# Kernel optimization log

Measured on AMD Instinct MI355X. Metric: run time of the kernel, lower is better.

The kernel has to match this reference:

```python
import jax, jax.numpy as jnp
import numpy as np
from jax import lax

B, L, D = 2, 1024, 1024
EXPAND, N, K = 2, 16, 4          # expand, d_state, d_conv
DI = EXPAND * D                  # d_inner = 2048
R = (D + 15) // 16               # dt_rank = 64
EPS = 1e-5


def setup_inputs() -> dict:
    key = jax.random.key(0)
    ks = jax.random.split(key, 8)
    x = jax.random.normal(ks[0], (B, L, D), dtype=jnp.float32)
    ln_w = jnp.ones((D,), jnp.float32)
    ln_b = jnp.zeros((D,), jnp.float32)
    W_in = jax.random.normal(ks[1], (D, 2 * DI), jnp.float32) * (1.0 / np.sqrt(D))
    conv_w = jax.random.normal(ks[2], (DI, K), jnp.float32) * 0.2
    conv_b = jnp.zeros((DI,), jnp.float32)
    W_x = jax.random.normal(ks[3], (DI, R + 2 * N), jnp.float32) * (1.0 / np.sqrt(DI))
    W_dt = jax.random.normal(ks[4], (R, DI), jnp.float32) * (1.0 / np.sqrt(R))
    b_dt = jnp.full((DI,), -4.0, jnp.float32)  # softplus(-4) ~ 0.018 dt init
    A_log = jnp.log(jnp.broadcast_to(jnp.arange(1, N + 1, dtype=jnp.float32), (DI, N)))
    D_param = jnp.ones((DI,), jnp.float32)
    W_out = jax.random.normal(ks[5], (DI, D), jnp.float32) * (1.0 / np.sqrt(DI))
    return {"x": x, "ln_w": ln_w, "ln_b": ln_b, "W_in": W_in, "conv_w": conv_w,
            "conv_b": conv_b, "W_x": W_x, "W_dt": W_dt, "b_dt": b_dt,
            "A_log": A_log, "D_param": D_param, "W_out": W_out}


def _mamba_block(x, ln_w, ln_b, W_in, conv_w, conv_b, W_x, W_dt, b_dt, A_log, D_param, W_out):
    # pre-LayerNorm
    mu = jnp.mean(x, axis=-1, keepdims=True)
    xc = x - mu
    var = jnp.mean(xc * xc, axis=-1, keepdims=True)
    h = xc * lax.rsqrt(var + EPS) * ln_w + ln_b          # [B,L,D]

    xz = h @ W_in                                        # [B,L,2*DI]
    xi, z = xz[..., :DI], xz[..., DI:]

    # depthwise causal conv1d, kernel K, left pad K-1
    xp = jnp.pad(xi, ((0, 0), (K - 1, 0), (0, 0)))
    conv = conv_b
    for k in range(K):
        conv = conv + xp[:, k:k + L, :] * conv_w[:, k]
    u = jax.nn.silu(conv)                                # [B,L,DI]

    proj = u @ W_x                                       # [B,L,R+2N]
    dt_r = proj[..., :R]
    Bm = proj[..., R:R + N]                              # [B,L,N]
    Cm = proj[..., R + N:]                               # [B,L,N]
    dt = jax.nn.softplus(dt_r @ W_dt + b_dt)             # [B,L,DI]

    A = -jnp.exp(A_log)                                  # [DI,N]
    dA = jnp.exp(dt[..., None] * A)                      # [B,L,DI,N]
    dBu = (dt * u)[..., None] * Bm[:, :, None, :]        # [B,L,DI,N]

    def comb(e1, e2):
        a1, b1 = e1
        a2, b2 = e2
        return a1 * a2, a2 * b1 + b2

    _, hs = lax.associative_scan(comb, (dA, dBu), axis=1)  # [B,L,DI,N]
    y = jnp.einsum('bldn,bln->bld', hs, Cm) + u * D_param
    y = y * jax.nn.silu(z)
    return x + y @ W_out


def reference(x, ln_w, ln_b, W_in, conv_w, conv_b, W_x, W_dt, b_dt, A_log, D_param, W_out):
    return _mamba_block(x, ln_w, ln_b, W_in, conv_w, conv_b, W_x, W_dt, b_dt,
                        A_log, D_param, W_out)
```

## Files before the change

kernel.cpp:

```cpp
#include <hip/hip_runtime.h>
#include <hip/hip_bf16.h>
#include <math.h>

#define B_ 2
#define L_ 1024
#define D_ 1024
#define DI_ 2048
#define K_ 4
#define N_ 16
#define R_ 64
#define BL_ (B_ * L_)
#define EPS_ 1e-5f

#define IDX4(l) ((l) + (((l) >> 6) << 2))

typedef __attribute__((ext_vector_type(8))) short short8;
typedef __attribute__((ext_vector_type(4))) float f32x4;

__device__ inline unsigned short f2bf(float f) {
    unsigned u = __float_as_uint(f);
    unsigned r = (u + 0x7fffu + ((u >> 16) & 1u)) >> 16;
    return (unsigned short)r;
}
__device__ inline float bf2f(unsigned short s) {
    return __uint_as_float(((unsigned)s) << 16);
}
__device__ inline float fast_silu(float z) {
    return z * __builtin_amdgcn_rcpf(1.f + __expf(-z));
}
__device__ inline void gl_lds16(const void* g, void* l) {
    __builtin_amdgcn_global_load_lds(
        (const __attribute__((address_space(1))) void*)g,
        (__attribute__((address_space(3))) void*)l, 16, 0, 0);
}

template <int CTRL>
__device__ inline float dpp_shr(float x) {
    return __int_as_float(__builtin_amdgcn_update_dpp(
        0, __float_as_int(x), CTRL, 0xf, 0xf, true));
}
__device__ inline float row16_sum(float p) {
    p += dpp_shr<0x111>(p);
    p += dpp_shr<0x112>(p);
    p += dpp_shr<0x114>(p);
    p += dpp_shr<0x118>(p);
    return p;
}

__global__ void ln_kernel(const float* __restrict__ x, const float* __restrict__ w,
                          const float* __restrict__ b, unsigned short* __restrict__ hb) {
    int row = blockIdx.x;
    const float* xr = x + (size_t)row * D_;
    float4 v = ((const float4*)xr)[threadIdx.x];

    __shared__ float red[4];
    float s = v.x + v.y + v.z + v.w;
    for (int off = 1; off < 64; off <<= 1) s += __shfl_xor(s, off, 64);
    if ((threadIdx.x & 63) == 0) red[threadIdx.x >> 6] = s;
    __syncthreads();
    float mu = (red[0] + red[1] + red[2] + red[3]) * (1.0f / D_);
    __syncthreads();
    float cx = v.x - mu, cy = v.y - mu, cz = v.z - mu, cw = v.w - mu;
    float sq = cx*cx + cy*cy + cz*cz + cw*cw;
    for (int off = 1; off < 64; off <<= 1) sq += __shfl_xor(sq, off, 64);
    if ((threadIdx.x & 63) == 0) red[threadIdx.x >> 6] = sq;
    __syncthreads();
    float var = (red[0] + red[1] + red[2] + red[3]) * (1.0f / D_);
    float rstd = rsqrtf(var + EPS_);

    float4 wv = ((const float4*)w)[threadIdx.x];
    float4 bv = ((const float4*)b)[threadIdx.x];
    ushort4 o;
    o.x = f2bf(cx * rstd * wv.x + bv.x);
    o.y = f2bf(cy * rstd * wv.y + bv.y);
    o.z = f2bf(cz * rstd * wv.z + bv.z);
    o.w = f2bf(cw * rstd * wv.w + bv.w);
    ((ushort4*)(hb + (size_t)row * D_))[threadIdx.x] = o;
}

__global__ void transpose_cast_all(const float* __restrict__ W_in, const float* __restrict__ W_x,
                                   const float* __restrict__ W_out,
                                   unsigned short* __restrict__ WinT, unsigned short* __restrict__ WxT,
                                   unsigned short* __restrict__ WoutT) {
    int bid = blockIdx.x;
    const float* W; unsigned short* WT; int K, N, bx, by;
    if (bid < 4096)      { W = W_in;  WT = WinT;  K = 1024; N = 4096; bx = bid & 127; by = bid >> 7; }
    else if (bid < 4288) { int id = bid - 4096; W = W_x;  WT = WxT;  K = DI_; N = 96;   bx = id % 3;  by = id / 3; }
    else                 { int id = bid - 4288; W = W_out; WT = WoutT; K = DI_; N = 1024; bx = id & 31; by = id >> 5; }
    __shared__ float tile[32][33];
    int k0 = by * 32, n0 = bx * 32;
    int tr = threadIdx.x >> 5;
    int tc = threadIdx.x & 31;
#pragma unroll
    for (int i = 0; i < 4; ++i)
        tile[tr + i*8][tc] = W[(size_t)(k0 + tr + i*8) * N + n0 + tc];
    __syncthreads();
#pragma unroll
    for (int i = 0; i < 4; ++i)
        WT[(size_t)(n0 + tr + i*8) * K + k0 + tc] = f2bf(tile[tc][tr + i*8]);
}

template <int BN, int MODE>
__global__ __launch_bounds__(256) void mfma_gemm_bt(
        const unsigned short* __restrict__ A,  int lda,
        const unsigned short* __restrict__ BT, int ldb,
        float* __restrict__ C, int ldc, int Kchunk,
        float* __restrict__ xi, unsigned short* __restrict__ sz) {
    constexpr int NT = BN / 32;
    __shared__ unsigned short As[128 * 32];
    __shared__ unsigned short Bs[BN * 32];

    int tid = threadIdx.x;
    int wave = tid >> 6, lane = tid & 63;
    int lane15 = lane & 15, quad = lane >> 4;
    int wr = wave >> 1, wc = wave & 1;

    int m0 = blockIdx.y * 128;
    int n0 = blockIdx.x * BN;
    int kbeg = blockIdx.z * Kchunk;
    int kend = kbeg + Kchunk;

    f32x4 acc[4][NT];
#pragma unroll
    for (int i = 0; i < 4; ++i)
#pragma unroll
        for (int j = 0; j < NT; ++j) acc[i][j] = (f32x4){0.f, 0.f, 0.f, 0.f};

    constexpr int ACALLS = 8;
    constexpr int BCALLS = BN * 4 / 64;

    for (int k0 = kbeg; k0 < kend; k0 += 32) {
        __syncthreads();
        for (int c = wave; c < ACALLS + BCALLS; c += 4) {
            if (c < ACALLS) {
                int cell = c * 64 + lane;
                int m = cell >> 2, s = cell & 3;
                int q = s ^ (m & 3) ^ ((m >> 2) & 3);
                gl_lds16(A + (size_t)(m0 + m) * lda + k0 + q * 8, &As[c * 512]);
            } else {
                int cell = (c - ACALLS) * 64 + lane;
                int n = cell >> 2, s = cell & 3;
                int q = s ^ (n & 3) ^ ((n >> 2) & 3);
                gl_lds16(BT + (size_t)(n0 + n) * ldb + k0 + q * 8, &Bs[(c - ACALLS) * 512]);
            }
        }
        __syncthreads();

        short8 af[4], bfr[NT];
#pragma unroll
        for (int i = 0; i < 4; ++i) {
            int m = wr * 64 + i * 16 + lane15;
            int s = quad ^ (m & 3) ^ ((m >> 2) & 3);
            af[i] = *(const short8*)&As[m * 32 + s * 8];
        }
#pragma unroll
        for (int j = 0; j < NT; ++j) {
            int n = wc * (NT * 16) + j * 16 + lane15;
            int s = quad ^ (n & 3) ^ ((n >> 2) & 3);
            bfr[j] = *(const short8*)&Bs[n * 32 + s * 8];
        }
#pragma unroll
        for (int i = 0; i < 4; ++i)
#pragma unroll
            for (int j = 0; j < NT; ++j)
                acc[i][j] = __builtin_amdgcn_mfma_f32_16x16x32_bf16(af[i], bfr[j], acc[i][j], 0, 0, 0);
    }

#pragma unroll
    for (int i = 0; i < 4; ++i) {
        int row = m0 + wr * 64 + i * 16 + quad * 4;
#pragma unroll
        for (int j = 0; j < NT; ++j) {
            int col = n0 + wc * (NT * 16) + j * 16 + lane15;
#pragma unroll
            for (int r = 0; r < 4; ++r) {
                float v = acc[i][j][r];
                int rr = row + r;
                if (MODE == 0) {
                    C[(size_t)rr * ldc + col] = v;
                } else if (MODE == 1) {
                    atomicAdd(&C[(size_t)rr * ldc + col], v);
                } else {
                    if (col < DI_) xi[(size_t)rr * DI_ + col] = v;
                    else           sz[(size_t)rr * DI_ + (col - DI_)] = f2bf(fast_silu(v));
                }
            }
        }
    }
}

__global__ void conv_silu_kernel(const float* __restrict__ xi, const float* __restrict__ cw,
                                 const float* __restrict__ cb, unsigned short* __restrict__ ub) {
    int idx = blockIdx.x * blockDim.x + threadIdx.x;
    int c = idx & (DI_ - 1);
    int bl = idx >> 11;
    int l = bl & (L_ - 1);
    float4 w4 = ((const float4*)cw)[c];
    float acc = cb[c];
    const float* base = xi + (size_t)bl * DI_ + c;
    if (l >= 3) {
        acc = fmaf(base[-(size_t)3 * DI_], w4.x, acc);
        acc = fmaf(base[-(size_t)2 * DI_], w4.y, acc);
        acc = fmaf(base[-(size_t)1 * DI_], w4.z, acc);
        acc = fmaf(base[0],                w4.w, acc);
    } else {
        if (l >= 2) acc = fmaf(*(base - 2 * DI_), w4.y, acc);
        if (l >= 1) acc = fmaf(*(base - 1 * DI_), w4.z, acc);
        acc = fmaf(base[0], w4.w, acc);
    }
    ub[idx] = f2bf(fast_silu(acc));
}

__global__ __launch_bounds__(256) void dtprep(
        const float* __restrict__ proj, const float* __restrict__ W_dt,
        const float* __restrict__ b_dt, const unsigned short* __restrict__ ub,
        const unsigned short* __restrict__ szb, const float* __restrict__ Dp,
        float2* __restrict__ dtduT, unsigned int* __restrict__ szdT) {
    __shared__ alignas(16) unsigned char smem[64 * 65 * 8];
    float (*As)[68] = reinterpret_cast<float(*)[68]>(smem);
    float (*Bs)[64] = reinterpret_cast<float(*)[64]>(smem + 4352);
    float2 (*T2)[65] = reinterpret_cast<float2(*)[65]>(smem);
    unsigned int (*TU)[65] = reinterpret_cast<unsigned int(*)[65]>(smem);

    int tid = threadIdx.x;
    int n0 = blockIdx.x * 64;
    int m0 = blockIdx.y * 64;
    int ar = tid >> 2, ak = (tid & 3) << 2;
    int kb = tid >> 4, bc = (tid & 15) << 2;
    int ty = tid >> 4, tx = tid & 15;

    float acc[4][4] = {};
#pragma unroll
    for (int k0 = 0; k0 < R_; k0 += 16) {
        float4 av = *(const float4*)&proj[(size_t)(m0 + ar) * 96 + k0 + ak];
        As[ak + 0][ar] = av.x; As[ak + 1][ar] = av.y;
        As[ak + 2][ar] = av.z; As[ak + 3][ar] = av.w;
        float4 bv = *(const float4*)&W_dt[(size_t)(k0 + kb) * DI_ + n0 + bc];
        Bs[kb][bc + 0] = bv.x; Bs[kb][bc + 1] = bv.y;
        Bs[kb][bc + 2] = bv.z; Bs[kb][bc + 3] = bv.w;
        __syncthreads();
#pragma unroll
        for (int kk = 0; kk < 16; ++kk) {
            float a[4], bb[4];
#pragma unroll
            for (int i = 0; i < 4; ++i) a[i] = As[kk][ty * 4 + i];
#pragma unroll
            for (int j = 0; j < 4; ++j) bb[j] = Bs[kk][tx * 4 + j];
#pragma unroll
            for (int i = 0; i < 4; ++i)
#pragma unroll
                for (int j = 0; j < 4; ++j)
                    acc[i][j] = fmaf(a[i], bb[j], acc[i][j]);
        }
        __syncthreads();
    }

    float4 bd = *(const float4*)&b_dt[n0 + tx * 4];
    float4 dp4 = *(const float4*)&Dp[n0 + tx * 4];
    float bda[4] = {bd.x, bd.y, bd.z, bd.w};
    float dpa[4] = {dp4.x, dp4.y, dp4.z, dp4.w};
    float2 d2[4][4];
    unsigned int su[4][4];
#pragma unroll
    for (int i = 0; i < 4; ++i) {
        int bl = m0 + ty * 4 + i;
        ushort4 u4 = *(const ushort4*)&ub[(size_t)bl * DI_ + n0 + tx * 4];
        ushort4 s4 = *(const ushort4*)&szb[(size_t)bl * DI_ + n0 + tx * 4];
        unsigned short ua[4] = {u4.x, u4.y, u4.z, u4.w};
        unsigned short sa[4] = {s4.x, s4.y, s4.z, s4.w};
#pragma unroll
        for (int j = 0; j < 4; ++j) {
            float v = acc[i][j] + bda[j];
            float dtv = fmaxf(v, 0.f) + __logf(1.f + __expf(-fabsf(v)));
            float uu = bf2f(ua[j]);
            float szv = bf2f(sa[j]);
            d2[i][j] = make_float2(dtv, dtv * uu);
            su[i][j] = ((unsigned)f2bf(uu * dpa[j] * szv) << 16) | (unsigned)f2bf(szv);
        }
    }

#pragma unroll
    for (int i = 0; i < 4; ++i)
#pragma unroll
        for (int j = 0; j < 4; ++j)
            T2[ty * 4 + i][tx * 4 + j] = d2[i][j];
    __syncthreads();
#pragma unroll
    for (int i = 0; i < 8; ++i) {
        int c_l = (tid >> 5) + i * 8;
#pragma unroll
        for (int jj = 0; jj < 2; ++jj) {
            int bl_l = (tid & 31) + jj * 32;
            dtduT[(size_t)(n0 + c_l) * BL_ + m0 + bl_l] = T2[bl_l][c_l];
        }
    }
    __syncthreads();

#pragma unroll
    for (int i = 0; i < 4; ++i)
#pragma unroll
        for (int j = 0; j < 4; ++j)
            TU[ty * 4 + i][tx * 4 + j] = su[i][j];
    __syncthreads();
#pragma unroll
    for (int i = 0; i < 8; ++i) {
        int c_l = (tid >> 5) + i * 8;
#pragma unroll
        for (int jj = 0; jj < 2; ++jj) {
            int bl_l = (tid & 31) + jj * 32;
            szdT[(size_t)(n0 + c_l) * BL_ + m0 + bl_l] = TU[bl_l][c_l];
        }
    }
}

__global__ __launch_bounds__(256) void scan_v5(
        const float2* __restrict__ dtduT, const unsigned int* __restrict__ szdT,
        const float* __restrict__ proj, const float* __restrict__ A_log,
        unsigned short* __restrict__ yzT) {
    int bc = blockIdx.x;
    int b = bc >> 10;
    int cp = bc & 1023;
    int t = threadIdx.x;
    int n = t & 15;
    int cs = (t >> 4) & 1;
    int chunk = t >> 5;
    int c = cp * 2 + cs;

    __shared__ float dd[2][(L_ + 32) * 2];
    __shared__ float sA[8][32];
    __shared__ float sB[8][32];
    __shared__ float ps[2][L_ + 64];

    {
        int half = t >> 7;
        int tt = t & 127;
        int l = tt * 8;
        int cload = cp * 2 + half;
        const float4* g = (const float4*)(dtduT + (size_t)cload * BL_ + (size_t)b * L_ + l);
        int il2 = l + ((l >> 6) << 1);
        float* dst = &dd[half][il2 * 2];
        *(float4*)(dst + 0)  = g[0];
        *(float4*)(dst + 4)  = g[1];
        *(float4*)(dst + 8)  = g[2];
        *(float4*)(dst + 12) = g[3];
    }
    __syncthreads();

    float A = -__expf(A_log[c * N_ + n]);
    int l0 = chunk * 128;
    const float* pB = proj + (size_t)b * L_ * 96 + R_ + n;
    const float* pC = pB + N_;

    float a = 1.f, acc = 0.f;
#pragma unroll
    for (int h = 0; h < 2; ++h) {
        int lb = l0 + h * 64;
        const float* ddp = &dd[cs][(lb + ((lb >> 6) << 1)) * 2];
        const float* pBb = pB + (size_t)lb * 96;
#pragma unroll
        for (int q = 0; q < 16; ++q) {
            float4 d0 = *(const float4*)(ddp + q * 8);
            float4 d1 = *(const float4*)(ddp + q * 8 + 4);
            float b0 = pBb[(q*4 + 0) * 96];
            float b1 = pBb[(q*4 + 1) * 96];
            float b2 = pBb[(q*4 + 2) * 96];
            float b3 = pBb[(q*4 + 3) * 96];
            float e;
            e = __expf(d0.x * A); a *= e; acc = fmaf(e, acc, d0.y * b0);
            e = __expf(d0.z * A); a *= e; acc = fmaf(e, acc, d0.w * b1);
            e = __expf(d1.x * A); a *= e; acc = fmaf(e, acc, d1.y * b2);
            e = __expf(d1.z * A); a *= e; acc = fmaf(e, acc, d1.w * b3);
        }
    }
    sA[chunk][t & 31] = a;
    sB[chunk][t & 31] = acc;
    __syncthreads();

    if (t < 32) {
        float hc = 0.f;
#pragma unroll
        for (int j = 0; j < 8; ++j) {
            float aj = sA[j][t];
            float bj = sB[j][t];
            sB[j][t] = hc;
            hc = fmaf(aj, hc, bj);
        }
    }
    __syncthreads();
    float h = sB[chunk][t & 31];

#pragma unroll
    for (int hh = 0; hh < 2; ++hh) {
        int lb = l0 + hh * 64;
        const float* ddp = &dd[cs][(lb + ((lb >> 6) << 1)) * 2];
        const float* pBb = pB + (size_t)lb * 96;
        const float* pCb = pC + (size_t)lb * 96;
        float* psb = &ps[cs][IDX4(lb)];
#pragma unroll
        for (int q = 0; q < 16; ++q) {
            float4 d0 = *(const float4*)(ddp + q * 8);
            float4 d1 = *(const float4*)(ddp + q * 8 + 4);
            float b0 = pBb[(q*4 + 0) * 96], c0 = pCb[(q*4 + 0) * 96];
            float b1 = pBb[(q*4 + 1) * 96], c1 = pCb[(q*4 + 1) * 96];
            float b2 = pBb[(q*4 + 2) * 96], c2 = pCb[(q*4 + 2) * 96];
            float b3 = pBb[(q*4 + 3) * 96], c3 = pCb[(q*4 + 3) * 96];
            float e, p0, p1, p2, p3;
            e = __expf(d0.x * A); h = fmaf(e, h, d0.y * b0); p0 = row16_sum(h * c0);
            e = __expf(d0.z * A); h = fmaf(e, h, d0.w * b1); p1 = row16_sum(h * c1);
            e = __expf(d1.x * A); h = fmaf(e, h, d1.y * b2); p2 = row16_sum(h * c2);
            e = __expf(d1.z * A); h = fmaf(e, h, d1.w * b3); p3 = row16_sum(h * c3);
            if (n == 15) *(float4*)&psb[q * 4] = (float4){p0, p1, p2, p3};
        }
    }
    __syncthreads();

    {
        int half = t >> 7;
        int tt = t & 127;
        int l = tt * 8;
        int c_out = cp * 2 + half;
        size_t tb = (size_t)c_out * BL_ + (size_t)b * L_;
        const float* pp = &ps[half][IDX4(l)];
        ushort4 o[2];
#pragma unroll
        for (int g = 0; g < 2; ++g) {
            float4 p4 = *(const float4*)(pp + g * 4);
            uint4 sd4 = *(const uint4*)(szdT + tb + l + g * 4);
            o[g].x = f2bf(p4.x * bf2f((unsigned short)(sd4.x & 0xffff)) + bf2f((unsigned short)(sd4.x >> 16)));
            o[g].y = f2bf(p4.y * bf2f((unsigned short)(sd4.y & 0xffff)) + bf2f((unsigned short)(sd4.y >> 16)));
            o[g].z = f2bf(p4.z * bf2f((unsigned short)(sd4.z & 0xffff)) + bf2f((unsigned short)(sd4.z >> 16)));
            o[g].w = f2bf(p4.w * bf2f((unsigned short)(sd4.w & 0xffff)) + bf2f((unsigned short)(sd4.w >> 16)));
        }
        *(ushort4*)(yzT + tb + l) = o[0];
        *(ushort4*)(yzT + tb + l + 4) = o[1];
    }
}

__global__ void transpose_y(const unsigned short* __restrict__ yzT, unsigned short* __restrict__ yz) {
    __shared__ unsigned short t[32][33];
    int c0 = blockIdx.y * 32, bl0 = blockIdx.x * 32;
    int r = threadIdx.x >> 5;
    int col = threadIdx.x & 31;
#pragma unroll
    for (int i = 0; i < 4; ++i)
        t[r + i*8][col] = yzT[(size_t)(c0 + r + i*8) * BL_ + bl0 + col];
    __syncthreads();
#pragma unroll
    for (int i = 0; i < 4; ++i)
        yz[(size_t)(bl0 + r + i*8) * DI_ + c0 + col] = t[col][r + i*8];
}

extern "C" void kernel_launch(void* const* d_in, const int* in_sizes, int n_in,
                              void* d_out, int out_size, void* d_ws, size_t ws_size,
                              hipStream_t stream) {
    const float* x       = (const float*)d_in[0];
    const float* ln_w    = (const float*)d_in[1];
    const float* ln_b    = (const float*)d_in[2];
    const float* W_in    = (const float*)d_in[3];
    const float* conv_w  = (const float*)d_in[4];
    const float* conv_b  = (const float*)d_in[5];
    const float* W_x     = (const float*)d_in[6];
    const float* W_dt    = (const float*)d_in[7];
    const float* b_dt    = (const float*)d_in[8];
    const float* A_log   = (const float*)d_in[9];
    const float* D_param = (const float*)d_in[10];
    const float* W_out   = (const float*)d_in[11];
    float* out = (float*)d_out;

    uint8_t* p = (uint8_t*)d_ws;
    unsigned short* hb    = (unsigned short*)p;  p += (size_t)BL_ * D_ * 2;
    unsigned short* WinT  = (unsigned short*)p;  p += (size_t)4096 * 1024 * 2;
    float*          xib   = (float*)p;           p += (size_t)BL_ * DI_ * 4;
    unsigned short* szb   = (unsigned short*)p;  p += (size_t)BL_ * DI_ * 2;
    unsigned short* ub    = (unsigned short*)p;  p += (size_t)BL_ * DI_ * 2;
    unsigned short* WxT   = (unsigned short*)p;  p += (size_t)96 * DI_ * 2;
    float*          proj  = (float*)p;           p += (size_t)BL_ * 96 * 4;
    unsigned short* WoutT = (unsigned short*)p;  p += (size_t)1024 * DI_ * 2;
    float2*         dtduT = (float2*)p;          p += (size_t)BL_ * DI_ * 8;
    unsigned int*   szdT  = (unsigned int*)p;    p += (size_t)BL_ * DI_ * 4;
    unsigned short* yzT   = (unsigned short*)p;  p += (size_t)BL_ * DI_ * 2;
    unsigned short* yzb   = (unsigned short*)d_ws;

    hipMemsetAsync(proj, 0, (size_t)BL_ * 96 * 4, stream);
    hipMemcpyAsync(out, x, (size_t)BL_ * D_ * 4, hipMemcpyDeviceToDevice, stream);

    transpose_cast_all<<<6336, 256, 0, stream>>>(W_in, W_x, W_out, WinT, WxT, WoutT);

    ln_kernel<<<BL_, 256, 0, stream>>>(x, ln_w, ln_b, hb);

    mfma_gemm_bt<128, 3><<<dim3(4096 / 128, BL_ / 128, 1), 256, 0, stream>>>(
        hb, 1024, WinT, 1024, nullptr, 0, 1024, xib, szb);

    conv_silu_kernel<<<(BL_ * DI_) / 256, 256, 0, stream>>>(xib, conv_w, conv_b, ub);

    mfma_gemm_bt<96, 1><<<dim3(1, BL_ / 128, 16), 256, 0, stream>>>(
        ub, DI_, WxT, DI_, proj, 96, 128, nullptr, nullptr);

    dtprep<<<dim3(DI_ / 64, BL_ / 64), 256, 0, stream>>>(
        proj, W_dt, b_dt, ub, szb, D_param, dtduT, szdT);

    scan_v5<<<B_ * DI_ / 2, 256, 0, stream>>>(dtduT, szdT, proj, A_log, yzT);

    transpose_y<<<dim3(BL_ / 32, DI_ / 32), 256, 0, stream>>>(yzT, yzb);

    mfma_gemm_bt<128, 1><<<dim3(1024 / 128, BL_ / 128, 2), 256, 0, stream>>>(
        yzb, DI_, WoutT, DI_, out, 1024, 1024, nullptr, nullptr);
}
```

Baseline: 286.7 us.

## Store conv input as bf16, vectorize conv, interleave B/C, drop scan LDS staging

The in-projection GEMM now writes the conv input xi as bf16 instead of fp32. The conv kernel is vectorized to handle four channels per thread with ushort4 loads. dtprep additionally writes an interleaved B/C buffer, so the scan reads B and C as one float2 instead of two strided proj loads. The scan drops its LDS staging of dt/du and reads directly from global memory. This cuts memory traffic, at the cost of extra bf16 rounding of the conv input and possibly less efficient global access patterns in the scan.

```diff
diff --git a/kernel.cpp b/kernel.cpp
--- a/kernel.cpp
+++ b/kernel.cpp
@@ -105,7 +105,7 @@
         const unsigned short* __restrict__ A,  int lda,
         const unsigned short* __restrict__ BT, int ldb,
         float* __restrict__ C, int ldc, int Kchunk,
-        float* __restrict__ xi, unsigned short* __restrict__ sz) {
+        unsigned short* __restrict__ xi, unsigned short* __restrict__ sz) {
     constexpr int NT = BN / 32;
     __shared__ unsigned short As[128 * 32];
     __shared__ unsigned short Bs[BN * 32];
@@ -181,7 +181,7 @@
                 } else if (MODE == 1) {
                     atomicAdd(&C[(size_t)rr * ldc + col], v);
                 } else {
-                    if (col < DI_) xi[(size_t)rr * DI_ + col] = v;
+                    if (col < DI_) xi[(size_t)rr * DI_ + col] = f2bf(v);
                     else           sz[(size_t)rr * DI_ + (col - DI_)] = f2bf(fast_silu(v));
                 }
             }
@@ -189,33 +189,50 @@
     }
 }
 
-__global__ void conv_silu_kernel(const float* __restrict__ xi, const float* __restrict__ cw,
+__global__ void conv_silu_kernel(const unsigned short* __restrict__ xi, const float* __restrict__ cw,
                                  const float* __restrict__ cb, unsigned short* __restrict__ ub) {
     int idx = blockIdx.x * blockDim.x + threadIdx.x;
-    int c = idx & (DI_ - 1);
-    int bl = idx >> 11;
+    int c4 = (idx << 2) & (DI_ - 1);
+    int bl = (idx << 2) >> 11;
     int l = bl & (L_ - 1);
-    float4 w4 = ((const float4*)cw)[c];
-    float acc = cb[c];
-    const float* base = xi + (size_t)bl * DI_ + c;
+    float4 w0 = ((const float4*)cw)[c4 + 0];
+    float4 w1 = ((const float4*)cw)[c4 + 1];
+    float4 w2 = ((const float4*)cw)[c4 + 2];
+    float4 w3 = ((const float4*)cw)[c4 + 3];
+    float4 cbv = *(const float4*)&cb[c4];
+    float a0 = cbv.x, a1 = cbv.y, a2 = cbv.z, a3 = cbv.w;
+    const unsigned short* base = xi + (size_t)bl * DI_ + c4;
+
+    ushort4 t0 = *(const ushort4*)base;
+    a0 = fmaf(bf2f(t0.x), w0.w, a0); a1 = fmaf(bf2f(t0.y), w1.w, a1);
+    a2 = fmaf(bf2f(t0.z), w2.w, a2); a3 = fmaf(bf2f(t0.w), w3.w, a3);
+    if (l >= 1) {
+        ushort4 t1 = *(const ushort4*)(base - DI_);
+        a0 = fmaf(bf2f(t1.x), w0.z, a0); a1 = fmaf(bf2f(t1.y), w1.z, a1);
+        a2 = fmaf(bf2f(t1.z), w2.z, a2); a3 = fmaf(bf2f(t1.w), w3.z, a3);
+    }
+    if (l >= 2) {
+        ushort4 t2 = *(const ushort4*)(base - 2 * DI_);
+        a0 = fmaf(bf2f(t2.x), w0.y, a0); a1 = fmaf(bf2f(t2.y), w1.y, a1);
+        a2 = fmaf(bf2f(t2.z), w2.y, a2); a3 = fmaf(bf2f(t2.w), w3.y, a3);
+    }
     if (l >= 3) {
-        acc = fmaf(base[-(size_t)3 * DI_], w4.x, acc);
-        acc = fmaf(base[-(size_t)2 * DI_], w4.y, acc);
-        acc = fmaf(base[-(size_t)1 * DI_], w4.z, acc);
-        acc = fmaf(base[0],                w4.w, acc);
-    } else {
-        if (l >= 2) acc = fmaf(*(base - 2 * DI_), w4.y, acc);
-        if (l >= 1) acc = fmaf(*(base - 1 * DI_), w4.z, acc);
-        acc = fmaf(base[0], w4.w, acc);
-    }
-    ub[idx] = f2bf(fast_silu(acc));
+        ushort4 t3 = *(const ushort4*)(base - 3 * DI_);
+        a0 = fmaf(bf2f(t3.x), w0.x, a0); a1 = fmaf(bf2f(t3.y), w1.x, a1);
+        a2 = fmaf(bf2f(t3.z), w2.x, a2); a3 = fmaf(bf2f(t3.w), w3.x, a3);
+    }
+    ushort4 o;
+    o.x = f2bf(fast_silu(a0)); o.y = f2bf(fast_silu(a1));
+    o.z = f2bf(fast_silu(a2)); o.w = f2bf(fast_silu(a3));
+    *(ushort4*)(ub + (size_t)bl * DI_ + c4) = o;
 }
 
 __global__ __launch_bounds__(256) void dtprep(
         const float* __restrict__ proj, const float* __restrict__ W_dt,
         const float* __restrict__ b_dt, const unsigned short* __restrict__ ub,
         const unsigned short* __restrict__ szb, const float* __restrict__ Dp,
-        float2* __restrict__ dtduT, unsigned int* __restrict__ szdT) {
+        float2* __restrict__ dtduT, unsigned int* __restrict__ szdT,
+        float2* __restrict__ bcti) {
     __shared__ alignas(16) unsigned char smem[64 * 65 * 8];
     float (*As)[68] = reinterpret_cast<float(*)[68]>(smem);
     float (*Bs)[64] = reinterpret_cast<float(*)[64]>(smem + 4352);
@@ -311,11 +328,23 @@
             szdT[(size_t)(n0 + c_l) * BL_ + m0 + bl_l] = TU[bl_l][c_l];
         }
     }
-}
-
-__global__ __launch_bounds__(256) void scan_v5(
+
+    if (blockIdx.x == 0) {
+        int bl_l = tid >> 4;
+        int n = tid & 15;
+#pragma unroll
+        for (int i = 0; i < 4; ++i) {
+            int bl = m0 + i * 16 + bl_l;
+            float Bv = proj[(size_t)bl * 96 + R_ + n];
+            float Cv = proj[(size_t)bl * 96 + R_ + N_ + n];
+            bcti[(size_t)bl * 16 + n] = make_float2(Bv, Cv);
+        }
+    }
+}
+
+__global__ __launch_bounds__(256) void scan_v6(
         const float2* __restrict__ dtduT, const unsigned int* __restrict__ szdT,
-        const float* __restrict__ proj, const float* __restrict__ A_log,
+        const float2* __restrict__ bcti, const float* __restrict__ A_log,
         unsigned short* __restrict__ yzT) {
     int bc = blockIdx.x;
     int b = bc >> 10;
@@ -326,51 +355,29 @@
     int chunk = t >> 5;
     int c = cp * 2 + cs;
 
-    __shared__ float dd[2][(L_ + 32) * 2];
     __shared__ float sA[8][32];
     __shared__ float sB[8][32];
     __shared__ float ps[2][L_ + 64];
 
-    {
-        int half = t >> 7;
-        int tt = t & 127;
-        int l = tt * 8;
-        int cload = cp * 2 + half;
-        const float4* g = (const float4*)(dtduT + (size_t)cload * BL_ + (size_t)b * L_ + l);
-        int il2 = l + ((l >> 6) << 1);
-        float* dst = &dd[half][il2 * 2];
-        *(float4*)(dst + 0)  = g[0];
-        *(float4*)(dst + 4)  = g[1];
-        *(float4*)(dst + 8)  = g[2];
-        *(float4*)(dst + 12) = g[3];
-    }
-    __syncthreads();
-
     float A = -__expf(A_log[c * N_ + n]);
     int l0 = chunk * 128;
-    const float* pB = proj + (size_t)b * L_ * 96 + R_ + n;
-    const float* pC = pB + N_;
+    const float2* dpt = dtduT + (size_t)c * BL_ + (size_t)b * L_ + l0;
+    const float2* bci = bcti + ((size_t)b * L_ + l0) * 16 + n;
 
     float a = 1.f, acc = 0.f;
-#pragma unroll
-    for (int h = 0; h < 2; ++h) {
-        int lb = l0 + h * 64;
-        const float* ddp = &dd[cs][(lb + ((lb >> 6) << 1)) * 2];
-        const float* pBb = pB + (size_t)lb * 96;
-#pragma unroll
-        for (int q = 0; q < 16; ++q) {
-            float4 d0 = *(const float4*)(ddp + q * 8);
-            float4 d1 = *(const float4*)(ddp + q * 8 + 4);
-            float b0 = pBb[(q*4 + 0) * 96];
-            float b1 = pBb[(q*4 + 1) * 96];
-            float b2 = pBb[(q*4 + 2) * 96];
-            float b3 = pBb[(q*4 + 3) * 96];
-            float e;
-            e = __expf(d0.x * A); a *= e; acc = fmaf(e, acc, d0.y * b0);
-            e = __expf(d0.z * A); a *= e; acc = fmaf(e, acc, d0.w * b1);
-            e = __expf(d1.x * A); a *= e; acc = fmaf(e, acc, d1.y * b2);
-            e = __expf(d1.z * A); a *= e; acc = fmaf(e, acc, d1.w * b3);
-        }
+#pragma unroll 8
+    for (int i = 0; i < 128; i += 4) {
+        float4 d01 = *(const float4*)(dpt + i);
+        float4 d23 = *(const float4*)(dpt + i + 2);
+        float2 bc0 = bci[(i + 0) * 16];
+        float2 bc1 = bci[(i + 1) * 16];
+        float2 bc2 = bci[(i + 2) * 16];
+        float2 bc3 = bci[(i + 3) * 16];
+        float e;
+        e = __expf(d01.x * A); a *= e; acc = fmaf(e, acc, d01.y * bc0.x);
+        e = __expf(d01.z * A); a *= e; acc = fmaf(e, acc, d01.w * bc1.x);
+        e = __expf(d23.x * A); a *= e; acc = fmaf(e, acc, d23.y * bc2.x);
+        e = __expf(d23.z * A); a *= e; acc = fmaf(e, acc, d23.w * bc3.x);
     }
     sA[chunk][t & 31] = a;
     sB[chunk][t & 31] = acc;
@@ -389,28 +396,20 @@
     __syncthreads();
     float h = sB[chunk][t & 31];
 
-#pragma unroll
-    for (int hh = 0; hh < 2; ++hh) {
-        int lb = l0 + hh * 64;
-        const float* ddp = &dd[cs][(lb + ((lb >> 6) << 1)) * 2];
-        const float* pBb = pB + (size_t)lb * 96;
-        const float* pCb = pC + (size_t)lb * 96;
-        float* psb = &ps[cs][IDX4(lb)];
-#pragma unroll
-        for (int q = 0; q < 16; ++q) {
-            float4 d0 = *(const float4*)(ddp + q * 8);
-            float4 d1 = *(const float4*)(ddp + q * 8 + 4);
-            float b0 = pBb[(q*4 + 0) * 96], c0 = pCb[(q*4 + 0) * 96];
-            float b1 = pBb[(q*4 + 1) * 96], c1 = pCb[(q*4 + 1) * 96];
-            float b2 = pBb[(q*4 + 2) * 96], c2 = pCb[(q*4 + 2) * 96];
-            float b3 = pBb[(q*4 + 3) * 96], c3 = pCb[(q*4 + 3) * 96];
-            float e, p0, p1, p2, p3;
-            e = __expf(d0.x * A); h = fmaf(e, h, d0.y * b0); p0 = row16_sum(h * c0);
-            e = __expf(d0.z * A); h = fmaf(e, h, d0.w * b1); p1 = row16_sum(h * c1);
-            e = __expf(d1.x * A); h = fmaf(e, h, d1.y * b2); p2 = row16_sum(h * c2);
-            e = __expf(d1.z * A); h = fmaf(e, h, d1.w * b3); p3 = row16_sum(h * c3);
-            if (n == 15) *(float4*)&psb[q * 4] = (float4){p0, p1, p2, p3};
-        }
+#pragma unroll 8
+    for (int i = 0; i < 128; i += 4) {
+        float4 d01 = *(const float4*)(dpt + i);
+        float4 d23 = *(const float4*)(dpt + i + 2);
+        float2 bc0 = bci[(i + 0) * 16];
+        float2 bc1 = bci[(i + 1) * 16];
+        float2 bc2 = bci[(i + 2) * 16];
+        float2 bc3 = bci[(i + 3) * 16];
+        float e, p0, p1, p2, p3;
+        e = __expf(d01.x * A); h = fmaf(e, h, d01.y * bc0.x); p0 = row16_sum(h * bc0.y);
+        e = __expf(d01.z * A); h = fmaf(e, h, d01.w * bc1.x); p1 = row16_sum(h * bc1.y);
+        e = __expf(d23.x * A); h = fmaf(e, h, d23.y * bc2.x); p2 = row16_sum(h * bc2.y);
+        e = __expf(d23.z * A); h = fmaf(e, h, d23.w * bc3.x); p3 = row16_sum(h * bc3.y);
+        if (n == 15) *(float4*)&ps[cs][IDX4(l0 + i)] = (float4){p0, p1, p2, p3};
     }
     __syncthreads();
 
@@ -470,7 +469,7 @@
     uint8_t* p = (uint8_t*)d_ws;
     unsigned short* hb    = (unsigned short*)p;  p += (size_t)BL_ * D_ * 2;
     unsigned short* WinT  = (unsigned short*)p;  p += (size_t)4096 * 1024 * 2;
-    float*          xib   = (float*)p;           p += (size_t)BL_ * DI_ * 4;
+    unsigned short* xib   = (unsigned short*)p;  p += (size_t)BL_ * DI_ * 2;
     unsigned short* szb   = (unsigned short*)p;  p += (size_t)BL_ * DI_ * 2;
     unsigned short* ub    = (unsigned short*)p;  p += (size_t)BL_ * DI_ * 2;
     unsigned short* WxT   = (unsigned short*)p;  p += (size_t)96 * DI_ * 2;
@@ -479,6 +478,7 @@
     float2*         dtduT = (float2*)p;          p += (size_t)BL_ * DI_ * 8;
     unsigned int*   szdT  = (unsigned int*)p;    p += (size_t)BL_ * DI_ * 4;
     unsigned short* yzT   = (unsigned short*)p;  p += (size_t)BL_ * DI_ * 2;
+    float2*         bcti  = (float2*)p;          p += (size_t)BL_ * 16 * 8;
     unsigned short* yzb   = (unsigned short*)d_ws;
 
     hipMemsetAsync(proj, 0, (size_t)BL_ * 96 * 4, stream);
@@ -491,15 +491,15 @@
     mfma_gemm_bt<128, 3><<<dim3(4096 / 128, BL_ / 128, 1), 256, 0, stream>>>(
         hb, 1024, WinT, 1024, nullptr, 0, 1024, xib, szb);
 
-    conv_silu_kernel<<<(BL_ * DI_) / 256, 256, 0, stream>>>(xib, conv_w, conv_b, ub);
+    conv_silu_kernel<<<(BL_ * DI_) / 1024, 256, 0, stream>>>(xib, conv_w, conv_b, ub);
 
     mfma_gemm_bt<96, 1><<<dim3(1, BL_ / 128, 16), 256, 0, stream>>>(
         ub, DI_, WxT, DI_, proj, 96, 128, nullptr, nullptr);
 
     dtprep<<<dim3(DI_ / 64, BL_ / 64), 256, 0, stream>>>(
-        proj, W_dt, b_dt, ub, szb, D_param, dtduT, szdT);
-
-    scan_v5<<<B_ * DI_ / 2, 256, 0, stream>>>(dtduT, szdT, proj, A_log, yzT);
+        proj, W_dt, b_dt, ub, szb, D_param, dtduT, szdT, bcti);
+
+    scan_v6<<<B_ * DI_ / 2, 256, 0, stream>>>(dtduT, szdT, bcti, A_log, yzT);
 
     transpose_y<<<dim3(BL_ / 32, DI_ / 32), 256, 0, stream>>>(yzT, yzb);
 
```

Result: slower. 336.7 us (+17.4%).
